# Optimization experiments

Hardware: AMD Instinct MI355X
Metric: run time of the kernel (lower is better)

The kernel has to match this reference:

```python
import jax, jax.numpy as jnp
import numpy as np
from jax import lax

WS = 8      # window size (square)
SS = 4      # shift size
HEADS = 8
K = 9       # snake-conv kernel size
CENTER = K // 2
EXT = 1.0   # extend_scope


def _shift_attn_mask(H, W):
    # static numpy construction of Swin shift mask -> [num_windows, L, L]
    m = np.zeros((H, W), dtype=np.float32)
    cnt = 0
    for hs in [(0, -WS), (-WS, -SS), (-SS, None)]:
        for ws_ in [(0, -WS), (-WS, -SS), (-SS, None)]:
            m[hs[0]:hs[1], ws_[0]:ws_[1]] = cnt
            cnt += 1
    m = m.reshape(H // WS, WS, W // WS, WS).transpose(0, 2, 1, 3).reshape(-1, WS * WS)
    d = m[:, None, :] - m[:, :, None]
    return jnp.asarray(np.where(d != 0, -100.0, 0.0).astype(np.float32))


def shifted_window_attention(x, qkv_w, qkv_b, proj_w, proj_b, rel_bias):
    B, H, W, C = x.shape
    d = C // HEADS
    x = jnp.roll(x, shift=(-SS, -SS), axis=(1, 2))
    nH, nW = H // WS, W // WS
    nwin, L = nH * nW, WS * WS
    # window partition -> [B*nwin, L, C]
    xw = x.reshape(B, nH, WS, nW, WS, C).transpose(0, 1, 3, 2, 4, 5).reshape(B * nwin, L, C)
    qkv = (xw @ qkv_w.T + qkv_b).reshape(B * nwin, L, 3, HEADS, d).transpose(2, 0, 3, 1, 4)
    q, k, v = qkv[0] * (d ** -0.5), qkv[1], qkv[2]
    attn = jnp.einsum('nhld,nhmd->nhlm', q, k) + rel_bias[None]
    amask = _shift_attn_mask(H, W)  # [nwin, L, L]
    attn = attn.reshape(B, nwin, HEADS, L, L) + amask[None, :, None]
    attn = jax.nn.softmax(attn.reshape(B * nwin, HEADS, L, L), axis=-1)
    out = jnp.einsum('nhlm,nhmd->nhld', attn, v).transpose(0, 2, 1, 3).reshape(B * nwin, L, C)
    out = out @ proj_w.T + proj_b
    out = out.reshape(B, nH, nW, WS, WS, C).transpose(0, 1, 3, 2, 4, 5).reshape(B, H, W, C)
    return jnp.roll(out, shift=(SS, SS), axis=(1, 2))


def snake_coordinate_map(offset):
    # offset [B, 2K, Wd, Hd], morph=0: cumulative y offsets from the kernel center
    B, _, Wd, Hd = offset.shape
    y_off = offset[:, :K]
    # y_new[center]=0; y_new[center+i]=sum_{j=1..i} y_off[center+j]; mirror below
    up = jnp.cumsum(y_off[:, CENTER + 1:], axis=1)
    down = jnp.cumsum(y_off[:, :CENTER][:, ::-1], axis=1)[:, ::-1]
    y_cum = jnp.concatenate([down, jnp.zeros((B, 1, Wd, Hd), offset.dtype), up], axis=1)
    y_center = jnp.arange(Wd, dtype=offset.dtype)[None, None, :, None]
    y_new = y_center + EXT * y_cum                              # [B,K,Wd,Hd]
    x_spread = jnp.linspace(-CENTER, CENTER, K, dtype=offset.dtype)[None, :, None, None]
    x_center = jnp.arange(Hd, dtype=offset.dtype)[None, None, None, :]
    x_new = jnp.broadcast_to(x_center + x_spread, (B, K, Wd, Hd))
    # rearrange 'b k w h -> b (w k) h'
    y_map = y_new.transpose(0, 2, 1, 3).reshape(B, Wd * K, Hd)
    x_map = x_new.transpose(0, 2, 1, 3).reshape(B, Wd * K, Hd)
    return y_map, x_map


def bilinear_sample(feat, ymap, xmap):
    Hin, Win = feat.shape[-2], feat.shape[-1]
    y = jnp.clip(ymap, 0.0, Hin - 1.0)
    x = jnp.clip(xmap, 0.0, Win - 1.0)
    y0f, x0f = jnp.floor(y), jnp.floor(x)
    wy, wx = y - y0f, x - x0f
    y0 = y0f.astype(jnp.int32); x0 = x0f.astype(jnp.int32)
    y1 = jnp.minimum(y0 + 1, Hin - 1); x1 = jnp.minimum(x0 + 1, Win - 1)
    g = jax.vmap(lambda f, yy, xx: f[:, yy, xx])  # -> [B,C,Ho,Wo]
    v00 = g(feat, y0, x0); v01 = g(feat, y0, x1)
    v10 = g(feat, y1, x0); v11 = g(feat, y1, x1)
    wy = wy[:, None]; wx = wx[:, None]
    return v00 * (1 - wy) * (1 - wx) + v01 * (1 - wy) * wx + v10 * wy * (1 - wx) + v11 * wy * wx


def _forward(x, qkv_weight, qkv_bias, proj_weight, proj_bias, rel_bias, offset, dsc_weight, dsc_bias):
    y = shifted_window_attention(x, qkv_weight, qkv_bias, proj_weight, proj_bias, rel_bias)
    feat = y.transpose(0, 3, 1, 2)                      # NCHW
    ymap, xmap = snake_coordinate_map(offset)
    samp = bilinear_sample(feat, ymap, xmap)            # [B,C,H*K,W]
    out = lax.conv_general_dilated(samp, dsc_weight, window_strides=(K, 1), padding='VALID',
                                   dimension_numbers=('NCHW', 'OIHW', 'NCHW'))
    return jax.nn.relu(out + dsc_bias[None, :, None, None])


def setup_inputs() -> dict:
    key = jax.random.key(0)
    ks = jax.random.split(key, 9)
    B, H, W, C = 8, 64, 64, 256
    return {
        'x': jax.random.normal(ks[0], (B, H, W, C), jnp.float32),
        'qkv_weight': jax.random.normal(ks[1], (3 * C, C), jnp.float32) * 0.05,
        'qkv_bias': jax.random.normal(ks[2], (3 * C,), jnp.float32) * 0.05,
        'proj_weight': jax.random.normal(ks[3], (C, C), jnp.float32) * 0.05,
        'proj_bias': jax.random.normal(ks[4], (C,), jnp.float32) * 0.05,
        'rel_bias': jax.random.normal(ks[5], (HEADS, WS * WS, WS * WS), jnp.float32) * 0.05,
        'offset': jax.random.normal(ks[6], (B, 2 * K, H, W), jnp.float32),
        'dsc_weight': jax.random.normal(ks[7], (C, C, K, 1), jnp.float32) * 0.02,
        'dsc_bias': jax.random.normal(ks[8], (C,), jnp.float32) * 0.02,
    }


def reference(x, qkv_weight, qkv_bias, proj_weight, proj_bias, rel_bias, offset, dsc_weight, dsc_bias):
    return _forward(x, qkv_weight, qkv_bias, proj_weight, proj_bias, rel_bias, offset, dsc_weight, dsc_bias)
```

## Files before the change

### kernel.cpp

```cpp
#include <hip/hip_runtime.h>
#include <math.h>


#define NFLOAT_BUF 8388608

typedef float f32x4 __attribute__((ext_vector_type(4)));
typedef __bf16 bf16x8 __attribute__((ext_vector_type(8)));
typedef _Float16 f16x8 __attribute__((ext_vector_type(8)));

__device__ inline unsigned pack2_bf16(float a, float b) {
    union { float f; unsigned u; } ua, ub;
    ua.f = a; ub.f = b;
    unsigned ra = (ua.u + 0x7FFFu + ((ua.u >> 16) & 1u)) >> 16;
    unsigned rb = (ub.u + 0x7FFFu + ((ub.u >> 16) & 1u)) & 0xFFFF0000u;
    return (ra & 0xFFFFu) | rb;
}
__device__ inline unsigned short pack1_bf16(float a) {
    union { float f; unsigned u; } v;
    v.f = a;
    return (unsigned short)((v.u + 0x7FFFu + ((v.u >> 16) & 1u)) >> 16);
}

__global__ __launch_bounds__(256) void cvt_bf16_kernel(const float* __restrict__ src,
                                                       unsigned short* __restrict__ dst,
                                                       int n8) {
    int t = blockIdx.x * 256 + threadIdx.x;
    if (t >= n8) return;
    const float4* s = (const float4*)(src + (size_t)t * 8);
    float4 a = s[0], b = s[1];
    uint4 o;
    o.x = pack2_bf16(a.x, a.y); o.y = pack2_bf16(a.z, a.w);
    o.z = pack2_bf16(b.x, b.y); o.w = pack2_bf16(b.z, b.w);
    *(uint4*)(dst + (size_t)t * 8) = o;
}

__global__ __launch_bounds__(256) void transpose_w_kernel(const float* __restrict__ w,
                                                          _Float16* __restrict__ wT) {
    int t = blockIdx.x * 256 + threadIdx.x;
    int o = t / 2304;
    int kk = t - o * 2304;
    int k = kk >> 8, i = kk & 255;
    wT[t] = (_Float16)w[(o * 256 + i) * 9 + k];
}

__global__ __launch_bounds__(256) void ymap_kernel(const float* __restrict__ offset,
                                                   float* __restrict__ ymap) {
    int t = blockIdx.x * 256 + threadIdx.x;
    int hd = t & 63;
    int wd = (t >> 6) & 63;
    int b  = t >> 12;
    const float* op = offset + ((size_t)(b * 18) * 64 + wd) * 64 + hd;
    float yo[9];
    #pragma unroll
    for (int k = 0; k < 9; ++k) yo[k] = op[(size_t)k * 4096];
    float cum[9];
    cum[4] = 0.0f;
    float s = 0.0f;
    for (int j = 3; j >= 0; --j) { s += yo[j]; cum[j] = s; }
    s = 0.0f;
    for (int j = 5; j < 9; ++j) { s += yo[j]; cum[j] = s; }
    float wdf = (float)wd;
    float* yp = ymap + ((size_t)(b * 576 + wd * 9)) * 64 + hd;
    #pragma unroll
    for (int k = 0; k < 9; ++k) yp[(size_t)k * 64] = wdf + cum[k];
}

__global__ __launch_bounds__(256) void qkv_mfma_kernel(
    const unsigned short* __restrict__ xb, const unsigned short* __restrict__ wb,
    const float* __restrict__ qkv_b,
    _Float16* __restrict__ qh, _Float16* __restrict__ kh, _Float16* __restrict__ vt) {

    __shared__ __align__(16) char Asb[8192];
    __shared__ __align__(16) char Bsb[32768];
    __shared__ unsigned rowoff[64];

    int nb = blockIdx.x;
    int m0 = blockIdx.y * 64;
    int tid = threadIdx.x;
    int lane = tid & 63, w = tid >> 6;
    int gw = m0 >> 6;

    if (tid < 64) {
        int l = tid;
        int b = gw >> 6, win = gw & 63;
        int rh = ((win >> 3) << 3) + (l >> 3);
        int rw = ((win & 7) << 3) + (l & 7);
        int sh = (rh + 4) & 63, sw = (rw + 4) & 63;
        rowoff[l] = (unsigned)(((b * 64 + sh) * 64 + sw) * 512);
    }

    f32x4 acc[4][4];
    #pragma unroll
    for (int m = 0; m < 4; ++m)
        #pragma unroll
        for (int n = 0; n < 4; ++n) {
            f32x4 z = {0.0f, 0.0f, 0.0f, 0.0f};
            acc[m][n] = z;
        }

    const char* xc = (const char*)xb;
    const char* wc = (const char*)wb;
    int rA = (lane & 15) * 128;
    int u0 = (((lane >> 4)    ) ^ (lane & 7)) << 4;
    int u1 = ((4 + (lane >> 4)) ^ (lane & 7)) << 4;

    __syncthreads();

    for (int c = 0; c < 4; ++c) {
        #pragma unroll
        for (int r = 0; r < 2; ++r) {
            int pos = r * 256 + tid;
            int row = pos >> 3, u = pos & 7;
            const char* src = xc + rowoff[row] + c * 128 + ((u ^ (row & 7)) << 4);
            __builtin_amdgcn_global_load_lds(
                (const __attribute__((address_space(1))) unsigned int*)src,
                (__attribute__((address_space(3))) unsigned int*)(Asb + pos * 16),
                16, 0, 0);
        }
        #pragma unroll
        for (int r = 0; r < 8; ++r) {
            int pos = r * 256 + tid;
            int n = pos >> 3, u = pos & 7;
            const char* src = wc + (size_t)(nb * 256 + n) * 512 + c * 128 + ((u ^ (n & 7)) << 4);
            __builtin_amdgcn_global_load_lds(
                (const __attribute__((address_space(1))) unsigned int*)src,
                (__attribute__((address_space(3))) unsigned int*)(Bsb + pos * 16),
                16, 0, 0);
        }
        __syncthreads();

        bf16x8 av[4][2], bv[4][2];
        #pragma unroll
        for (int m = 0; m < 4; ++m) {
            av[m][0] = *(const bf16x8*)(Asb + m * 2048 + rA + u0);
            av[m][1] = *(const bf16x8*)(Asb + m * 2048 + rA + u1);
        }
        #pragma unroll
        for (int n = 0; n < 4; ++n) {
            bv[n][0] = *(const bf16x8*)(Bsb + w * 8192 + n * 2048 + rA + u0);
            bv[n][1] = *(const bf16x8*)(Bsb + w * 8192 + n * 2048 + rA + u1);
        }
        #pragma unroll
        for (int m = 0; m < 4; ++m)
            #pragma unroll
            for (int n = 0; n < 4; ++n) {
                acc[m][n] = __builtin_amdgcn_mfma_f32_16x16x32_bf16(av[m][0], bv[n][0], acc[m][n], 0, 0, 0);
                acc[m][n] = __builtin_amdgcn_mfma_f32_16x16x32_bf16(av[m][1], bv[n][1], acc[m][n], 0, 0, 0);
            }
        __syncthreads();
    }

    float scale = (nb == 0) ? 0.17677669529663689f : 1.0f;
    #pragma unroll
    for (int nf = 0; nf < 4; ++nf) {
        int o = w * 64 + nf * 16 + (lane & 15);
        float bias = qkv_b[nb * 256 + o];
        int hh = o >> 5, dd = o & 31;
        if (nb < 2) {
            _Float16* dstb = (nb == 0) ? qh : kh;
            _Float16* base = dstb + ((size_t)(gw * 8 + hh) * 64) * 32 + dd;
            #pragma unroll
            for (int mf = 0; mf < 4; ++mf) {
                int l0 = mf * 16 + (lane >> 4) * 4;
                #pragma unroll
                for (int j = 0; j < 4; ++j)
                    base[(size_t)(l0 + j) * 32] = (_Float16)((acc[mf][nf][j] + bias) * scale);
            }
        } else {
            _Float16* base = vt + ((size_t)(gw * 8 + hh) * 32 + dd) * 64;
            #pragma unroll
            for (int mf = 0; mf < 4; ++mf) {
                int l0 = mf * 16 + (lane >> 4) * 4;
                union { _Float16 x[4]; uint2 u; } pk;
                #pragma unroll
                for (int j = 0; j < 4; ++j) pk.x[j] = (_Float16)(acc[mf][nf][j] + bias);
                *(uint2*)(base + l0) = pk.u;
            }
        }
    }
}

__global__ __launch_bounds__(512) void attn_mfma_kernel(
    const _Float16* __restrict__ qh, const _Float16* __restrict__ kh,
    const _Float16* __restrict__ vt, const float* __restrict__ rel_bias,
    unsigned short* __restrict__ attn_ob) {

    __shared__ __align__(16) char Plds[65536];
    int n = blockIdx.x;
    int win = n & 63;
    int wy = win >> 3, wx = win & 7;
    int tid = threadIdx.x, lane = tid & 63, h = tid >> 6;
    int qc = lane & 15, g = lane >> 4;
    char* P = Plds + h * 8192;

    const _Float16* qp = qh + (size_t)(n * 8 + h) * 2048;
    const _Float16* kp = kh + (size_t)(n * 8 + h) * 2048;
    const _Float16* vp = vt + (size_t)(n * 8 + h) * 2048;
    const float* rb = rel_bias + (size_t)h * 4096;

    int rk[16];
    #pragma unroll
    for (int mt = 0; mt < 4; ++mt)
        #pragma unroll
        for (int j = 0; j < 4; ++j) {
            int key = mt * 16 + g * 4 + j;
            int rh = wy * 8 + (key >> 3), rw = wx * 8 + (key & 7);
            rk[mt * 4 + j] = (rh < 56 ? 0 : (rh < 60 ? 1 : 2)) * 3
                           + (rw < 56 ? 0 : (rw < 60 ? 1 : 2));
        }

    f16x8 kf[4];
    #pragma unroll
    for (int mt = 0; mt < 4; ++mt)
        kf[mt] = *(const f16x8*)(kp + (mt * 16 + qc) * 32 + g * 8);

    #pragma unroll
    for (int nt = 0; nt < 4; ++nt) {
        int q = nt * 16 + qc;
        int rqh = wy * 8 + (q >> 3), rqw = wx * 8 + (q & 7);
        int rq = (rqh < 56 ? 0 : (rqh < 60 ? 1 : 2)) * 3
               + (rqw < 56 ? 0 : (rqw < 60 ? 1 : 2));
        f16x8 qf = *(const f16x8*)(qp + q * 32 + g * 8);

        f32x4 s[4];
        #pragma unroll
        for (int mt = 0; mt < 4; ++mt) {
            f32x4 z = {0.0f, 0.0f, 0.0f, 0.0f};
            s[mt] = __builtin_amdgcn_mfma_f32_16x16x32_f16(kf[mt], qf, z, 0, 0, 0);
        }

        float vals[16];
        #pragma unroll
        for (int mt = 0; mt < 4; ++mt) {
            float4 bv4 = *(const float4*)(rb + q * 64 + mt * 16 + g * 4);
            vals[mt * 4 + 0] = s[mt][0] + bv4.x + (rk[mt * 4 + 0] != rq ? -100.0f : 0.0f);
            vals[mt * 4 + 1] = s[mt][1] + bv4.y + (rk[mt * 4 + 1] != rq ? -100.0f : 0.0f);
            vals[mt * 4 + 2] = s[mt][2] + bv4.z + (rk[mt * 4 + 2] != rq ? -100.0f : 0.0f);
            vals[mt * 4 + 3] = s[mt][3] + bv4.w + (rk[mt * 4 + 3] != rq ? -100.0f : 0.0f);
        }

        float mx = vals[0];
        #pragma unroll
        for (int i = 1; i < 16; ++i) mx = fmaxf(mx, vals[i]);
        mx = fmaxf(mx, __shfl_xor(mx, 16));
        mx = fmaxf(mx, __shfl_xor(mx, 32));

        float sum = 0.0f;
        #pragma unroll
        for (int i = 0; i < 16; ++i) { vals[i] = __expf(vals[i] - mx); sum += vals[i]; }
        sum += __shfl_xor(sum, 16);
        sum += __shfl_xor(sum, 32);
        float inv = 1.0f / sum;

        #pragma unroll
        for (int mt = 0; mt < 4; ++mt) {
            union { _Float16 x[4]; uint2 u; } pk4;
            #pragma unroll
            for (int j = 0; j < 4; ++j) pk4.x[j] = (_Float16)(vals[mt * 4 + j] * inv);
            int off = (mt * 32 + g * 8) ^ ((q & 7) << 4);
            *(uint2*)(P + q * 128 + off) = pk4.u;
        }
    }

    f16x8 pa[4][2];
    #pragma unroll
    for (int im = 0; im < 4; ++im)
        #pragma unroll
        for (int ks = 0; ks < 2; ++ks) {
            int row = im * 16 + qc;
            int off = (ks * 64 + g * 16) ^ ((row & 7) << 4);
            pa[im][ks] = *(const f16x8*)(P + row * 128 + off);
        }
    f16x8 bvv[2][2];
    #pragma unroll
    for (int in = 0; in < 2; ++in)
        #pragma unroll
        for (int ks = 0; ks < 2; ++ks)
            bvv[in][ks] = *(const f16x8*)(vp + (in * 16 + qc) * 64 + ks * 32 + g * 8);

    f32x4 acc[4][2];
    #pragma unroll
    for (int im = 0; im < 4; ++im)
        #pragma unroll
        for (int in = 0; in < 2; ++in) {
            f32x4 z = {0.0f, 0.0f, 0.0f, 0.0f};
            acc[im][in] = z;
        }
    #pragma unroll
    for (int im = 0; im < 4; ++im)
        #pragma unroll
        for (int in = 0; in < 2; ++in) {
            acc[im][in] = __builtin_amdgcn_mfma_f32_16x16x32_f16(pa[im][0], bvv[in][0], acc[im][in], 0, 0, 0);
            acc[im][in] = __builtin_amdgcn_mfma_f32_16x16x32_f16(pa[im][1], bvv[in][1], acc[im][in], 0, 0, 0);
        }

    #pragma unroll
    for (int im = 0; im < 4; ++im)
        #pragma unroll
        for (int in = 0; in < 2; ++in)
            #pragma unroll
            for (int j = 0; j < 4; ++j) {
                int q2 = im * 16 + g * 4 + j;
                attn_ob[(size_t)(n * 64 + q2) * 256 + h * 32 + in * 16 + qc] =
                    pack1_bf16(acc[im][in][j]);
            }
}

__global__ __launch_bounds__(256) void proj_mfma_kernel(
    const unsigned short* __restrict__ attn_ob, const unsigned short* __restrict__ pwb,
    const float* __restrict__ proj_b, _Float16* __restrict__ feath) {

    __shared__ __align__(16) char Asb[8192];
    __shared__ __align__(16) char Bsb[32768];

    int m0 = blockIdx.x * 64;
    int tid = threadIdx.x;
    int lane = tid & 63, w = tid >> 6;
    int gw = m0 >> 6;
    int bidx = gw >> 6, win = gw & 63;

    f32x4 acc[4][4];
    #pragma unroll
    for (int m = 0; m < 4; ++m)
        #pragma unroll
        for (int n = 0; n < 4; ++n) {
            f32x4 z = {0.0f, 0.0f, 0.0f, 0.0f};
            acc[m][n] = z;
        }

    const char* ac = (const char*)attn_ob;
    const char* wc = (const char*)pwb;
    int rA = (lane & 15) * 128;
    int u0 = (((lane >> 4)    ) ^ (lane & 7)) << 4;
    int u1 = ((4 + (lane >> 4)) ^ (lane & 7)) << 4;

    for (int c = 0; c < 4; ++c) {
        #pragma unroll
        for (int r = 0; r < 2; ++r) {
            int pos = r * 256 + tid;
            int row = pos >> 3, u = pos & 7;
            const char* src = ac + (size_t)(m0 + row) * 512 + c * 128 + ((u ^ (row & 7)) << 4);
            __builtin_amdgcn_global_load_lds(
                (const __attribute__((address_space(1))) unsigned int*)src,
                (__attribute__((address_space(3))) unsigned int*)(Asb + pos * 16),
                16, 0, 0);
        }
        #pragma unroll
        for (int r = 0; r < 8; ++r) {
            int pos = r * 256 + tid;
            int n = pos >> 3, u = pos & 7;
            const char* src = wc + (size_t)n * 512 + c * 128 + ((u ^ (n & 7)) << 4);
            __builtin_amdgcn_global_load_lds(
                (const __attribute__((address_space(1))) unsigned int*)src,
                (__attribute__((address_space(3))) unsigned int*)(Bsb + pos * 16),
                16, 0, 0);
        }
        __syncthreads();

        bf16x8 av[4][2], bv[4][2];
        #pragma unroll
        for (int m = 0; m < 4; ++m) {
            av[m][0] = *(const bf16x8*)(Asb + m * 2048 + rA + u0);
            av[m][1] = *(const bf16x8*)(Asb + m * 2048 + rA + u1);
        }
        #pragma unroll
        for (int n = 0; n < 4; ++n) {
            bv[n][0] = *(const bf16x8*)(Bsb + w * 8192 + n * 2048 + rA + u0);
            bv[n][1] = *(const bf16x8*)(Bsb + w * 8192 + n * 2048 + rA + u1);
        }
        #pragma unroll
        for (int m = 0; m < 4; ++m)
            #pragma unroll
            for (int n = 0; n < 4; ++n) {
                acc[m][n] = __builtin_amdgcn_mfma_f32_16x16x32_bf16(av[m][0], bv[n][0], acc[m][n], 0, 0, 0);
                acc[m][n] = __builtin_amdgcn_mfma_f32_16x16x32_bf16(av[m][1], bv[n][1], acc[m][n], 0, 0, 0);
            }
        __syncthreads();
    }

    #pragma unroll
    for (int nf = 0; nf < 4; ++nf) {
        int f = w * 64 + nf * 16 + (lane & 15);
        float bias = proj_b[f];
        #pragma unroll
        for (int mf = 0; mf < 4; ++mf) {
            #pragma unroll
            for (int j = 0; j < 4; ++j) {
                int px = mf * 16 + (lane >> 4) * 4 + j;
                int rh = ((win >> 3) << 3) + (px >> 3);
                int rw = ((win & 7) << 3) + (px & 7);
                int p = (rh + 4) & 63;
                int qq = (rw + 4) & 63;
                feath[((size_t)(bidx * 64 + p) * 64 + qq) * 256 + f] =
                    (_Float16)(acc[mf][nf][j] + bias);
            }
        }
    }
}

__global__ __launch_bounds__(256) void sample_conv_mfma3_kernel(
    const _Float16* __restrict__ feath, const float* __restrict__ ymap,
    const _Float16* __restrict__ wT2h, const float* __restrict__ dsc_b,
    float* __restrict__ out) {

    __shared__ __align__(16) char Asb[8192];
    __shared__ __align__(16) char Bsb[32768];
    __shared__ unsigned row0[9][64];
    __shared__ unsigned row1[9][64];
    __shared__ float    wyv[9][64];

    int blk = blockIdx.x;
    int b = blk & 7, wd = blk >> 3;
    int tid = threadIdx.x;
    int lane = tid & 63, w = tid >> 6;
    int qc = lane & 15, g = lane >> 4;

    for (int idx = tid; idx < 576; idx += 256) {
        int k = idx >> 6, hd = idx & 63;
        float y = ymap[((size_t)(b * 576 + wd * 9 + k)) * 64 + hd];
        y = fminf(fmaxf(y, 0.0f), 63.0f);
        float y0f = floorf(y);
        int y0 = (int)y0f;
        int y1 = min(y0 + 1, 63);
        int xc = min(max(hd + k - 4, 0), 63);
        row0[k][hd] = (unsigned)(((b * 64 + y0) * 64 + xc) * 512);
        row1[k][hd] = (unsigned)(((b * 64 + y1) * 64 + xc) * 512);
        wyv[k][hd] = y - y0f;
    }

    f32x4 acc[4][4];
    #pragma unroll
    for (int m = 0; m < 4; ++m)
        #pragma unroll
        for (int n = 0; n < 4; ++n) {
            f32x4 z = {0.0f, 0.0f, 0.0f, 0.0f};
            acc[m][n] = z;
        }

    const char* featc = (const char*)feath;
    const char* wc    = (const char*)wT2h;

    int pxA0 = tid >> 3;
    int sA   = tid & 7;
    int rA = qc * 128;
    int u0 = ((g    ) ^ (lane & 7)) << 4;
    int u1 = ((4 + g) ^ (lane & 7)) << 4;

    __syncthreads();

    for (int c = 0; c < 36; ++c) {
        #pragma unroll
        for (int r = 0; r < 8; ++r) {
            int pos = r * 256 + tid;
            int n = pos >> 3, uu = pos & 7;
            int s = uu ^ (n & 7);
            const char* src = wc + n * 4608 + c * 128 + s * 16;
            __builtin_amdgcn_global_load_lds(
                (const __attribute__((address_space(1))) unsigned int*)src,
                (__attribute__((address_space(3))) unsigned int*)(Bsb + pos * 16),
                16, 0, 0);
        }
        int ks  = c >> 2;
        int cib = (c & 3) * 128;
        #pragma unroll
        for (int r = 0; r < 2; ++r) {
            int px = pxA0 + r * 32;
            unsigned b0 = row0[ks][px] + cib + sA * 16;
            unsigned b1 = row1[ks][px] + cib + sA * 16;
            float wy = wyv[ks][px];
            f16x8 v0 = *(const f16x8*)(featc + b0);
            f16x8 v1 = *(const f16x8*)(featc + b1);
            _Float16 wyh = (_Float16)wy;
            _Float16 omh = (_Float16)(1.0f - wy);
            f16x8 res = v0 * omh + v1 * wyh;
            *(f16x8*)(Asb + px * 128 + ((sA ^ (px & 7)) << 4)) = res;
        }
        __syncthreads();

        f16x8 av[4][2], bv[4][2];
        #pragma unroll
        for (int m = 0; m < 4; ++m) {
            av[m][0] = *(const f16x8*)(Asb + m * 2048 + rA + u0);
            av[m][1] = *(const f16x8*)(Asb + m * 2048 + rA + u1);
        }
        #pragma unroll
        for (int n = 0; n < 4; ++n) {
            bv[n][0] = *(const f16x8*)(Bsb + w * 8192 + n * 2048 + rA + u0);
            bv[n][1] = *(const f16x8*)(Bsb + w * 8192 + n * 2048 + rA + u1);
        }
        #pragma unroll
        for (int m = 0; m < 4; ++m)
            #pragma unroll
            for (int n = 0; n < 4; ++n) {
                acc[m][n] = __builtin_amdgcn_mfma_f32_16x16x32_f16(av[m][0], bv[n][0], acc[m][n], 0, 0, 0);
                acc[m][n] = __builtin_amdgcn_mfma_f32_16x16x32_f16(av[m][1], bv[n][1], acc[m][n], 0, 0, 0);
            }
        __syncthreads();
    }

    #pragma unroll
    for (int n = 0; n < 4; ++n) {
        int o = w * 64 + n * 16 + qc;
        float bvs = dsc_b[o];
        float* orow = out + ((size_t)(b * 256 + o) * 64 + wd) * 64;
        #pragma unroll
        for (int m = 0; m < 4; ++m) {
            int px = m * 16 + g * 4;
            float4 res;
            res.x = fmaxf(acc[m][n][0] + bvs, 0.0f);
            res.y = fmaxf(acc[m][n][1] + bvs, 0.0f);
            res.z = fmaxf(acc[m][n][2] + bvs, 0.0f);
            res.w = fmaxf(acc[m][n][3] + bvs, 0.0f);
            *(float4*)(orow + px) = res;
        }
    }
}

extern "C" void kernel_launch(void* const* d_in, const int* in_sizes, int n_in,
                              void* d_out, int out_size, void* d_ws, size_t ws_size,
                              hipStream_t stream) {
    (void)in_sizes; (void)n_in; (void)out_size; (void)ws_size;
    const float* x        = (const float*)d_in[0];
    const float* qkv_w    = (const float*)d_in[1];
    const float* qkv_b    = (const float*)d_in[2];
    const float* proj_w   = (const float*)d_in[3];
    const float* proj_b   = (const float*)d_in[4];
    const float* rel_bias = (const float*)d_in[5];
    const float* offset   = (const float*)d_in[6];
    const float* dsc_w    = (const float*)d_in[7];
    const float* dsc_b    = (const float*)d_in[8];
    float* out = (float*)d_out;

    unsigned short* wsu = (unsigned short*)d_ws;
    _Float16* qh = (_Float16*)wsu;
    _Float16* kh = (_Float16*)(wsu + NFLOAT_BUF);
    _Float16* vt = (_Float16*)(wsu + 2 * (size_t)NFLOAT_BUF);
    unsigned short* attn_ob = wsu + 3 * (size_t)NFLOAT_BUF;
    _Float16* feath = (_Float16*)(wsu + 4 * (size_t)NFLOAT_BUF);
    unsigned short* xb      = wsu + 5 * (size_t)NFLOAT_BUF;
    unsigned short* wb      = wsu + 6 * (size_t)NFLOAT_BUF;
    unsigned short* pwb     = wb + 196608;
    _Float16* wT2h          = (_Float16*)(pwb + 65536);
    float* ymap = (float*)((unsigned short*)wT2h + 589824);

    cvt_bf16_kernel<<<4096, 256, 0, stream>>>(x, xb, 1048576);
    cvt_bf16_kernel<<<96, 256, 0, stream>>>(qkv_w, wb, 24576);
    cvt_bf16_kernel<<<32, 256, 0, stream>>>(proj_w, pwb, 8192);
    transpose_w_kernel<<<2304, 256, 0, stream>>>(dsc_w, wT2h);
    ymap_kernel<<<128, 256, 0, stream>>>(offset, ymap);
    qkv_mfma_kernel<<<dim3(3, 512), 256, 0, stream>>>(xb, wb, qkv_b, qh, kh, vt);
    attn_mfma_kernel<<<512, 512, 0, stream>>>(qh, kh, vt, rel_bias, attn_ob);
    proj_mfma_kernel<<<512, 256, 0, stream>>>(attn_ob, pwb, proj_b, feath);
    sample_conv_mfma3_kernel<<<512, 256, 0, stream>>>(feath, ymap, wT2h, dsc_b, out);
}
```

Measured before the change: 227.4 us.

## Double-buffer sample-conv LDS tiles and process two output rows per block

The snake sample-conv kernel now covers two output rows per block with 512 threads, so each weight tile loaded into LDS feeds twice as many pixels. It also double-buffers the A and B tiles: the next chunk's weight loads and bilinear feature gathers are issued before the current MFMAs, and the interpolated result is written to the other buffer afterwards. This targets redundant weight traffic and exposed load latency. In exchange, LDS use rises to about 100KB per block and the grid shrinks to 256 blocks, which lowers occupancy and the number of blocks in flight.

```diff
diff --git a/kernel.cpp b/kernel.cpp
--- a/kernel.cpp
+++ b/kernel.cpp
@@ -398,34 +398,38 @@
     }
 }
 
-__global__ __launch_bounds__(256) void sample_conv_mfma3_kernel(
+__global__ __launch_bounds__(512) void sample_conv_mfma4_kernel(
     const _Float16* __restrict__ feath, const float* __restrict__ ymap,
     const _Float16* __restrict__ wT2h, const float* __restrict__ dsc_b,
     float* __restrict__ out) {
 
-    __shared__ __align__(16) char Asb[8192];
-    __shared__ __align__(16) char Bsb[32768];
-    __shared__ unsigned row0[9][64];
-    __shared__ unsigned row1[9][64];
-    __shared__ float    wyv[9][64];
+    __shared__ __align__(16) char Ab[2][16384];
+    __shared__ __align__(16) char Bb[2][32768];
+    __shared__ unsigned row0[2][9][64];
+    __shared__ unsigned row1[2][9][64];
+    __shared__ float    wyv[2][9][64];
 
     int blk = blockIdx.x;
-    int b = blk & 7, wd = blk >> 3;
+    int b = blk & 7, wd0 = (blk >> 3) * 2;
     int tid = threadIdx.x;
     int lane = tid & 63, w = tid >> 6;
     int qc = lane & 15, g = lane >> 4;
-
-    for (int idx = tid; idx < 576; idx += 256) {
-        int k = idx >> 6, hd = idx & 63;
+    int ph = w >> 2, nq = w & 3;
+
+    for (int idx = tid; idx < 1152; idx += 512) {
+        int wdl = idx / 576;
+        int r = idx - wdl * 576;
+        int k = r >> 6, hd = r & 63;
+        int wd = wd0 + wdl;
         float y = ymap[((size_t)(b * 576 + wd * 9 + k)) * 64 + hd];
         y = fminf(fmaxf(y, 0.0f), 63.0f);
         float y0f = floorf(y);
         int y0 = (int)y0f;
         int y1 = min(y0 + 1, 63);
         int xc = min(max(hd + k - 4, 0), 63);
-        row0[k][hd] = (unsigned)(((b * 64 + y0) * 64 + xc) * 512);
-        row1[k][hd] = (unsigned)(((b * 64 + y1) * 64 + xc) * 512);
-        wyv[k][hd] = y - y0f;
+        row0[wdl][k][hd] = (unsigned)(((b * 64 + y0) * 64 + xc) * 512);
+        row1[wdl][k][hd] = (unsigned)(((b * 64 + y1) * 64 + xc) * 512);
+        wyv[wdl][k][hd] = y - y0f;
     }
 
     f32x4 acc[4][4];
@@ -440,53 +444,88 @@
     const char* featc = (const char*)feath;
     const char* wc    = (const char*)wT2h;
 
-    int pxA0 = tid >> 3;
-    int sA   = tid & 7;
-    int rA = qc * 128;
-    int u0 = ((g    ) ^ (lane & 7)) << 4;
-    int u1 = ((4 + g) ^ (lane & 7)) << 4;
+    int pxA[2], sAv[2];
+    #pragma unroll
+    for (int r = 0; r < 2; ++r) {
+        int pos = r * 512 + tid;
+        pxA[r] = pos >> 3;
+        sAv[r] = pos & 7;
+    }
+
+    int rAa = qc * 128;
+    int u0 = ((g    ) ^ (qc & 7)) << 4;
+    int u1 = ((4 + g) ^ (qc & 7)) << 4;
 
     __syncthreads();
 
+    #pragma unroll
+    for (int r = 0; r < 4; ++r) {
+        int pos = r * 512 + tid;
+        int n = pos >> 3, uu = pos & 7;
+        const char* src = wc + n * 4608 + 0 * 128 + ((uu ^ (n & 7)) << 4);
+        __builtin_amdgcn_global_load_lds(
+            (const __attribute__((address_space(1))) unsigned int*)src,
+            (__attribute__((address_space(3))) unsigned int*)(Bb[0] + pos * 16),
+            16, 0, 0);
+    }
+    #pragma unroll
+    for (int r = 0; r < 2; ++r) {
+        int px = pxA[r], sA = sAv[r];
+        int wdl = px >> 6, hd = px & 63;
+        unsigned b0 = row0[wdl][0][hd] + sA * 16;
+        unsigned b1 = row1[wdl][0][hd] + sA * 16;
+        float wy = wyv[wdl][0][hd];
+        f16x8 v0 = *(const f16x8*)(featc + b0);
+        f16x8 v1 = *(const f16x8*)(featc + b1);
+        _Float16 wyh = (_Float16)wy;
+        _Float16 omh = (_Float16)(1.0f - wy);
+        f16x8 res = v0 * omh + v1 * wyh;
+        *(f16x8*)(Ab[0] + px * 128 + ((sA ^ (px & 7)) << 4)) = res;
+    }
+    __syncthreads();
+
     for (int c = 0; c < 36; ++c) {
-        #pragma unroll
-        for (int r = 0; r < 8; ++r) {
-            int pos = r * 256 + tid;
-            int n = pos >> 3, uu = pos & 7;
-            int s = uu ^ (n & 7);
-            const char* src = wc + n * 4608 + c * 128 + s * 16;
-            __builtin_amdgcn_global_load_lds(
-                (const __attribute__((address_space(1))) unsigned int*)src,
-                (__attribute__((address_space(3))) unsigned int*)(Bsb + pos * 16),
-                16, 0, 0);
-        }
-        int ks  = c >> 2;
-        int cib = (c & 3) * 128;
-        #pragma unroll
-        for (int r = 0; r < 2; ++r) {
-            int px = pxA0 + r * 32;
-            unsigned b0 = row0[ks][px] + cib + sA * 16;
-            unsigned b1 = row1[ks][px] + cib + sA * 16;
-            float wy = wyv[ks][px];
-            f16x8 v0 = *(const f16x8*)(featc + b0);
-            f16x8 v1 = *(const f16x8*)(featc + b1);
-            _Float16 wyh = (_Float16)wy;
-            _Float16 omh = (_Float16)(1.0f - wy);
-            f16x8 res = v0 * omh + v1 * wyh;
-            *(f16x8*)(Asb + px * 128 + ((sA ^ (px & 7)) << 4)) = res;
-        }
-        __syncthreads();
+        int cur = c & 1, nxt = cur ^ 1;
+
+        f16x8 s0[2], s1[2];
+        float swy[2];
+        if (c < 35) {
+            int cn = c + 1;
+            int ks = cn >> 2, cib = (cn & 3) * 128;
+            #pragma unroll
+            for (int r = 0; r < 4; ++r) {
+                int pos = r * 512 + tid;
+                int n = pos >> 3, uu = pos & 7;
+                const char* src = wc + n * 4608 + cn * 128 + ((uu ^ (n & 7)) << 4);
+                __builtin_amdgcn_global_load_lds(
+                    (const __attribute__((address_space(1))) unsigned int*)src,
+                    (__attribute__((address_space(3))) unsigned int*)(Bb[nxt] + pos * 16),
+                    16, 0, 0);
+            }
+            #pragma unroll
+            for (int r = 0; r < 2; ++r) {
+                int px = pxA[r], sA = sAv[r];
+                int wdl = px >> 6, hd = px & 63;
+                unsigned b0 = row0[wdl][ks][hd] + cib + sA * 16;
+                unsigned b1 = row1[wdl][ks][hd] + cib + sA * 16;
+                swy[r] = wyv[wdl][ks][hd];
+                s0[r] = *(const f16x8*)(featc + b0);
+                s1[r] = *(const f16x8*)(featc + b1);
+            }
+        }
 
         f16x8 av[4][2], bv[4][2];
         #pragma unroll
         for (int m = 0; m < 4; ++m) {
-            av[m][0] = *(const f16x8*)(Asb + m * 2048 + rA + u0);
-            av[m][1] = *(const f16x8*)(Asb + m * 2048 + rA + u1);
+            char* abase = Ab[cur] + ph * 8192 + m * 2048 + rAa;
+            av[m][0] = *(const f16x8*)(abase + u0);
+            av[m][1] = *(const f16x8*)(abase + u1);
         }
         #pragma unroll
         for (int n = 0; n < 4; ++n) {
-            bv[n][0] = *(const f16x8*)(Bsb + w * 8192 + n * 2048 + rA + u0);
-            bv[n][1] = *(const f16x8*)(Bsb + w * 8192 + n * 2048 + rA + u1);
+            char* bbase = Bb[cur] + nq * 8192 + n * 2048 + rAa;
+            bv[n][0] = *(const f16x8*)(bbase + u0);
+            bv[n][1] = *(const f16x8*)(bbase + u1);
         }
         #pragma unroll
         for (int m = 0; m < 4; ++m)
@@ -495,14 +534,25 @@
                 acc[m][n] = __builtin_amdgcn_mfma_f32_16x16x32_f16(av[m][0], bv[n][0], acc[m][n], 0, 0, 0);
                 acc[m][n] = __builtin_amdgcn_mfma_f32_16x16x32_f16(av[m][1], bv[n][1], acc[m][n], 0, 0, 0);
             }
+
+        if (c < 35) {
+            #pragma unroll
+            for (int r = 0; r < 2; ++r) {
+                int px = pxA[r], sA = sAv[r];
+                _Float16 wyh = (_Float16)swy[r];
+                _Float16 omh = (_Float16)(1.0f - swy[r]);
+                f16x8 res = s0[r] * omh + s1[r] * wyh;
+                *(f16x8*)(Ab[nxt] + px * 128 + ((sA ^ (px & 7)) << 4)) = res;
+            }
+        }
         __syncthreads();
     }
 
     #pragma unroll
     for (int n = 0; n < 4; ++n) {
-        int o = w * 64 + n * 16 + qc;
+        int o = nq * 64 + n * 16 + qc;
         float bvs = dsc_b[o];
-        float* orow = out + ((size_t)(b * 256 + o) * 64 + wd) * 64;
+        float* orow = out + ((size_t)(b * 256 + o) * 64 + (wd0 + ph)) * 64;
         #pragma unroll
         for (int m = 0; m < 4; ++m) {
             int px = m * 16 + g * 4;
@@ -551,5 +601,5 @@
     qkv_mfma_kernel<<<dim3(3, 512), 256, 0, stream>>>(xb, wb, qkv_b, qh, kh, vt);
     attn_mfma_kernel<<<512, 512, 0, stream>>>(qh, kh, vt, rel_bias, attn_ob);
     proj_mfma_kernel<<<512, 256, 0, stream>>>(attn_ob, pwb, proj_b, feath);
-    sample_conv_mfma3_kernel<<<512, 256, 0, stream>>>(feath, ymap, wT2h, dsc_b, out);
-}
+    sample_conv_mfma4_kernel<<<256, 512, 0, stream>>>(feath, ymap, wT2h, dsc_b, out);
+}
```

Measured after the change: 222.4 us. 1.02x faster.
